# Optimization experiments

Hardware: AMD Instinct MI355X
Metric: run time of the kernel (lower is better)

Reference implementation:

```python
import jax, jax.numpy as jnp
import numpy as np

B = 65536
HID = 256
C_K, C_V, C_S, NQ = 4, 8, 4, 4
EMB_OUT = 64  # state_embedding_size - 1


def _spatial_basis():
    # h = w = 5, U = V = 2 -> [5,5,4] Fourier basis
    ph = jnp.arange(1.0, 6.0)[:, None] * jnp.ones((1, 5)) * (np.pi / 5.0)
    pw = jnp.ones((5, 1)) * jnp.arange(1.0, 6.0)[None, :] * (np.pi / 5.0)
    u = jnp.arange(1.0, 3.0)[None, :]
    a = jnp.cos(ph[:, :, None] * u)  # [5,5,2]
    b = jnp.cos(pw[:, :, None] * u)  # [5,5,2]
    return jnp.einsum('hwu,hwv->hwuv', a, b).reshape(5, 5, 4).astype(jnp.float32)


def _conv(x, w, b):
    # x: NHWC, w: HWIO, pad=1, stride=1
    y = jax.lax.conv_general_dilated(x, w, window_strides=(1, 1), padding=[(1, 1), (1, 1)],
                                     dimension_numbers=('NHWC', 'HWIO', 'NHWC'))
    return y + b


def setup_inputs() -> dict:
    key = jax.random.key(0)
    ks = jax.random.split(key, 20)
    s = 0.05
    inp = {
        'X': jax.random.normal(ks[0], (B, 7, 7, 3), jnp.float32),
        'upper_module_hidden_state': jax.random.normal(ks[1], (B, HID), jnp.float32),
        'c1_w': jax.random.normal(ks[2], (5, 5, 3, 8), jnp.float32) * s,
        'c1_b': jax.random.normal(ks[3], (8,), jnp.float32) * s,
        'c2_w': jax.random.normal(ks[4], (3, 3, 8, 12), jnp.float32) * s,
        'c2_b': jax.random.normal(ks[5], (12,), jnp.float32) * s,
    }
    qdims = [(HID, 256), (256, 128), (128, 64), (64, 32), (32, 32)]
    for i, (din, dout) in enumerate(qdims):
        inp[f'qw{i}'] = jax.random.normal(ks[6 + 2 * i], (din, dout), jnp.float32) * s
        inp[f'qb{i}'] = jax.random.normal(ks[7 + 2 * i], (dout,), jnp.float32) * s
    inp['aw0'] = jax.random.normal(ks[16], ((C_V + C_S) * NQ, 32), jnp.float32) * s
    inp['ab0'] = jax.random.normal(ks[17], (32,), jnp.float32) * s
    inp['aw1'] = jax.random.normal(ks[18], (32, EMB_OUT), jnp.float32) * s
    inp['ab1'] = jax.random.normal(ks[19], (EMB_OUT,), jnp.float32) * s
    return inp


def reference(X, upper_module_hidden_state, c1_w, c1_b, c2_w, c2_b,
              qw0, qb0, qw1, qb1, qw2, qb2, qw3, qb3, qw4, qb4,
              aw0, ab0, aw1, ab1):
    b = X.shape[0]
    # vision CNN: [b,7,7,3] -> [b,5,5,8] -> [b,5,5,12]
    O = _conv(_conv(X, c1_w, c1_b), c2_w, c2_b)
    K, V = O[..., :C_K], O[..., C_K:]
    S = jnp.broadcast_to(_spatial_basis(), (b, 5, 5, C_S))
    K = jnp.concatenate([K, S], axis=-1)  # [b,5,5,8]
    V = jnp.concatenate([V, S], axis=-1)  # [b,5,5,12]
    # query MLP -> [b,4,8]
    q = upper_module_hidden_state
    for w, bi in [(qw0, qb0), (qw1, qb1), (qw2, qb2), (qw3, qb3)]:
        q = jax.nn.relu(q @ w + bi)
    q = (q @ qw4 + qb4).reshape(-1, NQ, C_K + C_S)
    # attention logits over 25 spatial positions, softmax over space
    A = jnp.einsum('bhwk,bqk->bhwq', K, q).reshape(b, 25, NQ)
    A = jax.nn.softmax(A, axis=1)
    # apply_alpha: [b,nq,25] @ [b,25,12] -> [b,nq,12]; chunk+cat == reshape
    a = jnp.einsum('bpq,bpd->bqd', A, V.reshape(b, 25, C_V + C_S)).reshape(b, NQ * (C_V + C_S))
    # answer MLP
    return jax.nn.relu(a @ aw0 + ab0) @ aw1 + ab1
```

## Files before the change

kernel.cpp:

```cpp
#include <hip/hip_runtime.h>
#include <hip/hip_bf16.h>

#define NB 65536

typedef __attribute__((ext_vector_type(8))) short short8;
typedef __attribute__((ext_vector_type(4))) short short4v;
typedef __attribute__((ext_vector_type(4))) float f32x4;
typedef __attribute__((ext_vector_type(16))) float f32x16;
typedef __attribute__((ext_vector_type(4))) unsigned int u32x4;

__device__ inline short f2bf(float f) {
    unsigned u = __builtin_bit_cast(unsigned, f);
    unsigned r = (u + 0x7fffu + ((u >> 16) & 1u)) >> 16;
    return (short)(unsigned short)r;
}
__device__ inline float b2f(short s) {
    return __builtin_bit_cast(float, (unsigned)((unsigned short)s) << 16);
}
__device__ inline unsigned pkbf(float lo, float hi) {
    return ((unsigned)(unsigned short)f2bf(hi) << 16) | (unsigned)(unsigned short)f2bf(lo);
}

#define MLPW_CNT 109568
#define WEFF_CNT 51200
#define A0 (MLPW_CNT + WEFF_CNT + 320)
#define A1 (A0 + 2048)
#define A2 (A1 + 2048)
#define A3 (A2 + 100)
#define PREP_TOT (A3 + 512)


__global__ void __launch_bounds__(256) prep_kernel(
    const float* __restrict__ w0, const float* __restrict__ w1,
    const float* __restrict__ w2, const float* __restrict__ w3,
    const float* __restrict__ w4,
    const float* __restrict__ b0, const float* __restrict__ b1,
    const float* __restrict__ b2, const float* __restrict__ b3,
    const float* __restrict__ b4,
    const float* __restrict__ c1w, const float* __restrict__ c1b,
    const float* __restrict__ c2w, const float* __restrict__ c2b,
    const float* __restrict__ aw0, const float* __restrict__ aw1,
    short* __restrict__ wt, short* __restrict__ weff, float* __restrict__ beff,
    short* __restrict__ aw0T, short* __restrict__ aw1T, float* __restrict__ sTab,
    float* __restrict__ biasP)
{
    int idx = blockIdx.x * 256 + threadIdx.x;
    if (idx < MLPW_CNT) {
        const float* W; int N, KT, base;
        if (idx < 65536)       { W = w0; N = 256; KT = 16; base = 0; }
        else if (idx < 98304)  { W = w1; N = 128; KT = 16; base = 65536; }
        else if (idx < 106496) { W = w2; N = 64;  KT = 8;  base = 98304; }
        else if (idx < 108544) { W = w3; N = 32;  KT = 4;  base = 106496; }
        else                   { W = w4; N = 32;  KT = 2;  base = 108544; }
        int i  = idx - base;
        int nt = i / (KT * 512);
        int r1 = i - nt * (KT * 512);
        int kt = r1 >> 9;
        int l  = (r1 & 511) >> 3;
        int j  = i & 7;
        int n  = nt * 32 + (l & 31);
        int k  = kt * 16 + ((l >> 5) << 3) + j;
        wt[idx] = f2bf(W[k * N + n]);
    } else if (idx < MLPW_CNT + WEFF_CNT) {
        int it = idx - MLPW_CNT;
        int n = it / 160, k = it - n * 160;
        float acc = 0.f;
        if (n < 300 && k < 147) {
            int oc = n % 12, p = n / 12, oy = p / 5, ox = p - oy * 5;
            int ci = k % 3,  t = k / 3, iy = t / 7, ix = t - iy * 7;
            for (int y = 0; y < 5; ++y) {
                int ky = iy - y + 1, ly = y - oy + 1;
                if ((unsigned)ky < 5u && (unsigned)ly < 3u) {
                    for (int x = 0; x < 5; ++x) {
                        int kx = ix - x + 1, lx = x - ox + 1;
                        if ((unsigned)kx < 5u && (unsigned)lx < 3u) {
                            const float* p1 = c1w + ((ky * 5 + kx) * 3 + ci) * 8;
                            const float* p2 = c2w + ((ly * 3 + lx) * 8) * 12 + oc;
#pragma unroll
                            for (int c = 0; c < 8; ++c) acc += p1[c] * p2[c * 12];
                        }
                    }
                }
            }
        }
        weff[it] = f2bf(acc);
    } else if (idx < A0) {
        int n = idx - MLPW_CNT - WEFF_CNT;
        float acc = 0.f;
        if (n < 300) {
            int oc = n % 12, p = n / 12, oy = p / 5, ox = p - oy * 5;
            acc = c2b[oc];
            for (int y = 0; y < 5; ++y) {
                int ly = y - oy + 1;
                if ((unsigned)ly < 3u) {
                    for (int x = 0; x < 5; ++x) {
                        int lx = x - ox + 1;
                        if ((unsigned)lx < 3u) {
#pragma unroll
                            for (int c = 0; c < 8; ++c)
                                acc += c2w[((ly * 3 + lx) * 8 + c) * 12 + oc] * c1b[c];
                        }
                    }
                }
            }
        }
        beff[n] = acc;
    } else if (idx < A1) {
        int t = idx - A0;
        int n = t >> 6, k = t & 63;
        aw0T[t] = (k < 48) ? f2bf(aw0[k * 32 + n]) : (short)0;
    } else if (idx < A2) {
        int t = idx - A1;
        int n = t >> 5, k = t & 31;
        aw1T[t] = f2bf(aw1[k * 64 + n]);
    } else if (idx < A3) {
        int i = idx - A2;
        int p = i >> 2, s = i & 3;
        int h = p / 5, w = p - 5 * h;
        int u = (s >> 1) + 1, v = (s & 1) + 1;
        const float PI5 = 0.6283185307179586f;
        sTab[i] = cosf(((float)(h + 1) * PI5) * (float)u) *
                  cosf(((float)(w + 1) * PI5) * (float)v);
    } else if (idx < PREP_TOT) {
        int t = idx - A3;
        const float* B; int N, base;
        if (t < 256)      { B = b0; N = 256; base = 0; }
        else if (t < 384) { B = b1; N = 128; base = 256; }
        else if (t < 448) { B = b2; N = 64;  base = 384; }
        else if (t < 480) { B = b3; N = 32;  base = 448; }
        else              { B = b4; N = 32;  base = 480; }
        int u  = t - base;
        int h  = u / (N / 2);
        int w  = u - h * (N / 2);
        int nt = w >> 4, r = w & 15;
        biasP[t] = B[nt * 32 + (r & 3) + 8 * (r >> 2) + 4 * h];
    }
}

template<int K, int N, bool RELU>
__device__ inline void layerR(const short* __restrict__ wp,
                              const float* __restrict__ bp,
                              const u32x4* __restrict__ inF,
                              u32x4* __restrict__ outF,
                              int lane, int h)
{
    constexpr int KT = K / 16, NT = N / 32;
#pragma unroll
    for (int nt = 0; nt < NT; ++nt) {
        f32x16 a;
#pragma unroll
        for (int r = 0; r < 16; ++r) a[r] = 0.f;
#pragma unroll
        for (int kt = 0; kt < KT; ++kt) {
            short8 wf = *(const short8*)(wp + (nt * KT + kt) * 512 + lane * 8);
            a = __builtin_amdgcn_mfma_f32_32x32x16_bf16(
                    wf, __builtin_bit_cast(short8, inF[kt]), a, 0, 0, 0);
        }
        const float* bpp = bp + h * (N / 2) + nt * 16;
        unsigned q[8];
#pragma unroll
        for (int i = 0; i < 8; ++i) {
            float v0 = a[2 * i] + bpp[2 * i];
            float v1 = a[2 * i + 1] + bpp[2 * i + 1];
            if (RELU) { v0 = fmaxf(v0, 0.f); v1 = fmaxf(v1, 0.f); }
            q[i] = pkbf(v0, v1);
        }
        unsigned xq[8];
#pragma unroll
        for (int i = 0; i < 8; ++i) xq[i] = (unsigned)__shfl_xor((int)q[i], 32, 64);
        u32x4 fa, fb;
        if (h == 0) {
            fa[0] = q[0];  fa[1] = q[1];  fa[2] = xq[0]; fa[3] = xq[1];
            fb[0] = q[4];  fb[1] = q[5];  fb[2] = xq[4]; fb[3] = xq[5];
        } else {
            fa[0] = xq[2]; fa[1] = xq[3]; fa[2] = q[2];  fa[3] = q[3];
            fb[0] = xq[6]; fb[1] = xq[7]; fb[2] = q[6];  fb[3] = q[7];
        }
        outF[2 * nt]     = fa;
        outF[2 * nt + 1] = fb;
    }
}

template<int K>
__device__ inline void layerQ(const short* __restrict__ wp,
                              const float* __restrict__ bp,
                              const u32x4* __restrict__ inF,
                              short* __restrict__ qout,
                              int lane, int h, int r0)
{
    constexpr int KT = K / 16;
    f32x16 a;
#pragma unroll
    for (int r = 0; r < 16; ++r) a[r] = 0.f;
#pragma unroll
    for (int kt = 0; kt < KT; ++kt) {
        short8 wf = *(const short8*)(wp + kt * 512 + lane * 8);
        a = __builtin_amdgcn_mfma_f32_32x32x16_bf16(
                wf, __builtin_bit_cast(short8, inF[kt]), a, 0, 0, 0);
    }
    const float* bpp = bp + h * 16;
    short* qb = qout + (size_t)(r0 + (lane & 31)) * 32 + 4 * h;
    const int fo[8] = {0, 2, 8, 10, 16, 18, 24, 26};
#pragma unroll
    for (int i = 0; i < 8; ++i) {
        float v0 = a[2 * i] + bpp[2 * i];
        float v1 = a[2 * i + 1] + bpp[2 * i + 1];
        *(unsigned*)(qb + fo[i]) = pkbf(v0, v1);
    }
}

__global__ void __launch_bounds__(64, 2) mlp_kernel(
    const float* __restrict__ hid,
    const short* __restrict__ wp,
    const float* __restrict__ biasP,
    short* __restrict__ qout)
{
    const int lane = threadIdx.x;
    const int h = lane >> 5, b = lane & 31;
    const int r0 = blockIdx.x * 32;

    u32x4 A[16], B[16], C[8], D[4], E[2];
    const float* hb = hid + (size_t)(r0 + b) * 256 + h * 8;
#pragma unroll
    for (int kt = 0; kt < 16; ++kt) {
        float4 x = *(const float4*)(hb + kt * 16);
        float4 y = *(const float4*)(hb + kt * 16 + 4);
        u32x4 f;
        f[0] = pkbf(x.x, x.y); f[1] = pkbf(x.z, x.w);
        f[2] = pkbf(y.x, y.y); f[3] = pkbf(y.z, y.w);
        A[kt] = f;
    }
    layerR<256, 256, true>(wp,          biasP,       A, B, lane, h);
    layerR<256, 128, true>(wp + 65536,  biasP + 256, B, C, lane, h);
    layerR<128,  64, true>(wp + 98304,  biasP + 384, C, D, lane, h);
    layerR< 64,  32, true>(wp + 106496, biasP + 448, D, E, lane, h);
    layerQ< 32>           (wp + 108544, biasP + 480, E, qout, lane, h, r0);
}

__global__ void __launch_bounds__(256, 4) conv_attn_kernel(
    const float* __restrict__ Xg,
    const short* __restrict__ weffT,
    const float* __restrict__ beff,
    const short* __restrict__ aw0T, const float* __restrict__ ab0,
    const short* __restrict__ aw1T, const float* __restrict__ ab1,
    const float* __restrict__ sTab,
    const short* __restrict__ qb16,
    float* __restrict__ out)
{
    __shared__ __align__(16) short sKV[4][4800];
    __shared__ __align__(16) short sA[4][1024];
    __shared__ __align__(16) short sH[4][512];

    const int tid    = threadIdx.x;
    const int w      = tid >> 6;
    const int lane   = tid & 63;
    const int lanelo = lane & 15;
    const int g      = lane >> 4;
    const int e0     = blockIdx.x * 64 + w * 16;

    short* sX  = &sKV[w][0];
    short* sKc = &sKV[w][0];
    short* sVc = &sKV[w][1600];

#pragma unroll
    for (int i = 0; i < 4; ++i) {
        int t = lane + i * 64;
        if (t < 208) {
            int r = t / 13, c = 147 + (t - r * 13);
            int ch = c >> 3;
            sX[r * 192 + ((ch ^ (r & 7)) << 3) + (c & 7)] = 0;
        }
    }
    {
        const float* xb = Xg + (size_t)e0 * 147;
#define PUTX(IDX, F) { int _i = (IDX); int _r = _i / 147; int _c = _i - _r * 147; \
        int _ch = _c >> 3; sX[_r * 192 + ((_ch ^ (_r & 7)) << 3) + (_c & 7)] = f2bf(F); }
#pragma unroll
        for (int i = 0; i < 10; ++i) {
            int idx4 = lane + i * 64;
            if (idx4 < 588) {
                float4 v = reinterpret_cast<const float4*>(xb)[idx4];
                int base = idx4 * 4;
                PUTX(base + 0, v.x)
                PUTX(base + 1, v.y)
                PUTX(base + 2, v.z)
                PUTX(base + 3, v.w)
            }
        }
#undef PUTX
    }

    short8 af[5];
#pragma unroll
    for (int kt = 0; kt < 5; ++kt) {
        int phys = (kt * 4 + g) ^ (lanelo & 7);
        af[kt] = *(const short8*)(sX + lanelo * 192 + phys * 8);
    }

    short8 bf[3][5];
    {
        const short* wb0 = weffT + lanelo * 160 + g * 8;
        const short* wb1 = weffT + (16 + lanelo) * 160 + g * 8;
#pragma unroll
        for (int kt = 0; kt < 5; ++kt) {
            bf[0][kt] = *(const short8*)(wb0 + kt * 32);
            bf[1][kt] = *(const short8*)(wb1 + kt * 32);
        }
    }
#pragma unroll
    for (int nt = 0; nt < 19; ++nt) {
        if (nt + 2 < 19) {
            const short* wb = weffT + ((nt + 2) * 16 + lanelo) * 160 + g * 8;
#pragma unroll
            for (int kt = 0; kt < 5; ++kt)
                bf[(nt + 2) % 3][kt] = *(const short8*)(wb + kt * 32);
        }
        f32x4 a; a[0] = 0.f; a[1] = 0.f; a[2] = 0.f; a[3] = 0.f;
#pragma unroll
        for (int kt = 0; kt < 5; ++kt)
            a = __builtin_amdgcn_mfma_f32_16x16x32_bf16(af[kt], bf[nt % 3][kt], a, 0, 0, 0);
        int n = nt * 16 + lanelo;
        if (n < 300) {
            float bb = beff[n];
            int p = n / 12, c = n - p * 12;
#pragma unroll
            for (int j = 0; j < 4; ++j) {
                int el = g * 4 + j;
                float v = a[j] + bb;
                if (c < 4) sKc[el * 100 + p * 4 + c]       = f2bf(v);
                else       sVc[el * 200 + p * 8 + (c - 4)] = f2bf(v);
            }
        }
    }

    {
        const int el = lane >> 2, qi = lane & 3;
        short8 qv = *(const short8*)(qb16 + (size_t)(e0 + el) * 32 + qi * 8);
        float qf[8];
#pragma unroll
        for (int i = 0; i < 8; ++i) qf[i] = b2f(qv[i]);

        float lg[25];
        float mx = -1e30f;
#pragma unroll
        for (int p = 0; p < 25; ++p) {
            short4v kv = *(const short4v*)(sKc + el * 100 + p * 4);
            float4 sv = *(const float4*)(sTab + p * 4);
            float s = b2f(kv[0]) * qf[0] + b2f(kv[1]) * qf[1]
                    + b2f(kv[2]) * qf[2] + b2f(kv[3]) * qf[3]
                    + sv.x * qf[4] + sv.y * qf[5]
                    + sv.z * qf[6] + sv.w * qf[7];
            lg[p] = s;
            mx = fmaxf(mx, s);
        }
        float sum = 0.f;
#pragma unroll
        for (int p = 0; p < 25; ++p) { lg[p] = __expf(lg[p] - mx); sum += lg[p]; }
        float inv = 1.f / sum;

        float o[12];
#pragma unroll
        for (int d = 0; d < 12; ++d) o[d] = 0.f;
#pragma unroll
        for (int p = 0; p < 25; ++p) {
            float wgt = lg[p];
            short4v v0 = *(const short4v*)(sVc + el * 200 + p * 8);
            short4v v1 = *(const short4v*)(sVc + el * 200 + p * 8 + 4);
            float4 sv = *(const float4*)(sTab + p * 4);
            o[0] += wgt * b2f(v0[0]); o[1] += wgt * b2f(v0[1]);
            o[2] += wgt * b2f(v0[2]); o[3] += wgt * b2f(v0[3]);
            o[4] += wgt * b2f(v1[0]); o[5] += wgt * b2f(v1[1]);
            o[6] += wgt * b2f(v1[2]); o[7] += wgt * b2f(v1[3]);
            o[8]  += wgt * sv.x; o[9]  += wgt * sv.y;
            o[10] += wgt * sv.z; o[11] += wgt * sv.w;
        }
#pragma unroll
        for (int d = 0; d < 12; ++d) {
            int col = qi * 12 + d;
            int ch = col >> 3;
            sA[w][el * 64 + ((ch ^ (el & 7)) << 3) + (col & 7)] = f2bf(o[d] * inv);
        }
#pragma unroll
        for (int z = 0; z < 4; ++z) {
            int col = 48 + qi * 4 + z;
            int ch = col >> 3;
            sA[w][el * 64 + ((ch ^ (el & 7)) << 3) + (col & 7)] = 0;
        }
    }

    {
        short8 aa0, aa1;
        {
            int p0 = (0 * 4 + g) ^ (lanelo & 7);
            int p1 = (1 * 4 + g) ^ (lanelo & 7);
            aa0 = *(const short8*)(&sA[w][0] + lanelo * 64 + p0 * 8);
            aa1 = *(const short8*)(&sA[w][0] + lanelo * 64 + p1 * 8);
        }
#pragma unroll
        for (int nt2 = 0; nt2 < 2; ++nt2) {
            int n = nt2 * 16 + lanelo;
            short8 bw0 = *(const short8*)(aw0T + n * 64 + g * 8);
            short8 bw1 = *(const short8*)(aw0T + n * 64 + 32 + g * 8);
            f32x4 hh; hh[0] = 0.f; hh[1] = 0.f; hh[2] = 0.f; hh[3] = 0.f;
            hh = __builtin_amdgcn_mfma_f32_16x16x32_bf16(aa0, bw0, hh, 0, 0, 0);
            hh = __builtin_amdgcn_mfma_f32_16x16x32_bf16(aa1, bw1, hh, 0, 0, 0);
            float bb = ab0[n];
#pragma unroll
            for (int j = 0; j < 4; ++j) {
                int row = g * 4 + j;
                int ch = n >> 3;
                float v = fmaxf(hh[j] + bb, 0.f);
                sH[w][row * 32 + ((ch ^ (row & 3)) << 3) + (n & 7)] = f2bf(v);
            }
        }
    }

    {
        short8 ah;
        {
            int ph = (g ^ (lanelo & 3));
            ah = *(const short8*)(&sH[w][0] + lanelo * 32 + ph * 8);
        }
#pragma unroll
        for (int nt3 = 0; nt3 < 4; ++nt3) {
            int n = nt3 * 16 + lanelo;
            short8 bw = *(const short8*)(aw1T + n * 32 + g * 8);
            f32x4 oacc; oacc[0] = 0.f; oacc[1] = 0.f; oacc[2] = 0.f; oacc[3] = 0.f;
            oacc = __builtin_amdgcn_mfma_f32_16x16x32_bf16(ah, bw, oacc, 0, 0, 0);
            float bb = ab1[n];
#pragma unroll
            for (int j = 0; j < 4; ++j) {
                int el = g * 4 + j;
                out[((size_t)e0 + el) * 64 + n] = oacc[j] + bb;
            }
        }
    }
}


extern "C" void kernel_launch(void* const* d_in, const int* in_sizes, int n_in,
                              void* d_out, int out_size, void* d_ws, size_t ws_size,
                              hipStream_t stream)
{
    const float* X   = (const float*)d_in[0];
    const float* hid = (const float*)d_in[1];
    const float* c1w = (const float*)d_in[2];
    const float* c1b = (const float*)d_in[3];
    const float* c2w = (const float*)d_in[4];
    const float* c2b = (const float*)d_in[5];
    const float* qw0 = (const float*)d_in[6];
    const float* qb0 = (const float*)d_in[7];
    const float* qw1 = (const float*)d_in[8];
    const float* qb1 = (const float*)d_in[9];
    const float* qw2 = (const float*)d_in[10];
    const float* qb2 = (const float*)d_in[11];
    const float* qw3 = (const float*)d_in[12];
    const float* qb3 = (const float*)d_in[13];
    const float* qw4 = (const float*)d_in[14];
    const float* qb4 = (const float*)d_in[15];
    const float* aw0 = (const float*)d_in[16];
    const float* ab0 = (const float*)d_in[17];
    const float* aw1 = (const float*)d_in[18];
    const float* ab1 = (const float*)d_in[19];

    float* out   = (float*)d_out;
    short* qb16  = (short*)d_ws;
    short* wsW   = qb16 + (size_t)NB * 32;
    short* weffT = wsW + MLPW_CNT;
    float* beff  = (float*)(weffT + WEFF_CNT);
    short* aw0T  = (short*)(beff + 320);
    short* aw1T  = aw0T + 2048;
    float* sTab  = (float*)(aw1T + 2048);
    float* biasP = sTab + 100;

    hipLaunchKernelGGL(prep_kernel, dim3((PREP_TOT + 255) / 256), dim3(256), 0, stream,
                       qw0, qw1, qw2, qw3, qw4, qb0, qb1, qb2, qb3, qb4,
                       c1w, c1b, c2w, c2b, aw0, aw1,
                       wsW, weffT, beff, aw0T, aw1T, sTab, biasP);
    hipLaunchKernelGGL(mlp_kernel, dim3(NB / 32), dim3(64), 0, stream,
                       hid, wsW, biasP, qb16);
    hipLaunchKernelGGL(conv_attn_kernel, dim3(NB / 64), dim3(256), 0, stream,
                       X, weffT, beff, aw0T, ab0, aw1T, ab1, sTab, qb16, out);
}
```

Measured before the change: 82.98 us.

## Fuse query MLP and conv-attention into one warp-specialized kernel

Merges the MLP kernel and the conv/attention kernel into a single 192-thread block. One wave computes the query MLP for 32 elements and writes the queries to shared memory, while two waves run the conv path, then all three sync before attention. This removes the global round trip of the query buffer and one kernel launch, and lets MLP and conv work overlap within a block. In exchange, the MLP wave sits idle after the sync, each block carries a heavier register footprint, and blocks are smaller, which may hurt occupancy.

```diff
diff --git a/kernel.cpp b/kernel.cpp
--- a/kernel.cpp
+++ b/kernel.cpp
@@ -185,8 +185,8 @@
 __device__ inline void layerQ(const short* __restrict__ wp,
                               const float* __restrict__ bp,
                               const u32x4* __restrict__ inF,
-                              short* __restrict__ qout,
-                              int lane, int h, int r0)
+                              short* qout,
+                              int lane, int h)
 {
     constexpr int KT = K / 16;
     f32x16 a;
@@ -199,7 +199,7 @@
                 wf, __builtin_bit_cast(short8, inF[kt]), a, 0, 0, 0);
     }
     const float* bpp = bp + h * 16;
-    short* qb = qout + (size_t)(r0 + (lane & 31)) * 32 + 4 * h;
+    short* qb = qout + (lane & 31) * 32 + 4 * h;
     const int fo[8] = {0, 2, 8, 10, 16, 18, 24, 26};
 #pragma unroll
     for (int i = 0; i < 8; ++i) {
@@ -209,58 +209,56 @@
     }
 }
 
-__global__ void __launch_bounds__(64, 2) mlp_kernel(
+__global__ void __launch_bounds__(192, 4) fused_kernel(
     const float* __restrict__ hid,
     const short* __restrict__ wp,
     const float* __restrict__ biasP,
-    short* __restrict__ qout)
-{
-    const int lane = threadIdx.x;
-    const int h = lane >> 5, b = lane & 31;
-    const int r0 = blockIdx.x * 32;
-
-    u32x4 A[16], B[16], C[8], D[4], E[2];
-    const float* hb = hid + (size_t)(r0 + b) * 256 + h * 8;
-#pragma unroll
-    for (int kt = 0; kt < 16; ++kt) {
-        float4 x = *(const float4*)(hb + kt * 16);
-        float4 y = *(const float4*)(hb + kt * 16 + 4);
-        u32x4 f;
-        f[0] = pkbf(x.x, x.y); f[1] = pkbf(x.z, x.w);
-        f[2] = pkbf(y.x, y.y); f[3] = pkbf(y.z, y.w);
-        A[kt] = f;
-    }
-    layerR<256, 256, true>(wp,          biasP,       A, B, lane, h);
-    layerR<256, 128, true>(wp + 65536,  biasP + 256, B, C, lane, h);
-    layerR<128,  64, true>(wp + 98304,  biasP + 384, C, D, lane, h);
-    layerR< 64,  32, true>(wp + 106496, biasP + 448, D, E, lane, h);
-    layerQ< 32>           (wp + 108544, biasP + 480, E, qout, lane, h, r0);
-}
-
-__global__ void __launch_bounds__(256, 4) conv_attn_kernel(
     const float* __restrict__ Xg,
     const short* __restrict__ weffT,
     const float* __restrict__ beff,
     const short* __restrict__ aw0T, const float* __restrict__ ab0,
     const short* __restrict__ aw1T, const float* __restrict__ ab1,
     const float* __restrict__ sTab,
-    const short* __restrict__ qb16,
     float* __restrict__ out)
 {
-    __shared__ __align__(16) short sKV[4][4800];
-    __shared__ __align__(16) short sA[4][1024];
-    __shared__ __align__(16) short sH[4][512];
-
-    const int tid    = threadIdx.x;
-    const int w      = tid >> 6;
-    const int lane   = tid & 63;
+    __shared__ __align__(16) short sPool[2][4800];
+    __shared__ __align__(16) short sQ[1024];
+
+    const int tid  = threadIdx.x;
+    const int w    = tid / 64;
+    const int lane = tid & 63;
+    const int e0   = blockIdx.x * 32;
+
+    if (w == 0) {
+        const int h = lane >> 5, b = lane & 31;
+        u32x4 A[16], B[16], C[8], D[4], E[2];
+        const float* hb = hid + (size_t)(e0 + b) * 256 + h * 8;
+#pragma unroll
+        for (int kt = 0; kt < 16; ++kt) {
+            float4 x = *(const float4*)(hb + kt * 16);
+            float4 y = *(const float4*)(hb + kt * 16 + 4);
+            u32x4 f;
+            f[0] = pkbf(x.x, x.y); f[1] = pkbf(x.z, x.w);
+            f[2] = pkbf(y.x, y.y); f[3] = pkbf(y.z, y.w);
+            A[kt] = f;
+        }
+        layerR<256, 256, true>(wp,          biasP,       A, B, lane, h);
+        layerR<256, 128, true>(wp + 65536,  biasP + 256, B, C, lane, h);
+        layerR<128,  64, true>(wp + 98304,  biasP + 384, C, D, lane, h);
+        layerR< 64,  32, true>(wp + 106496, biasP + 448, D, E, lane, h);
+        layerQ< 32>           (wp + 108544, biasP + 480, E, sQ, lane, h);
+        __syncthreads();
+        return;
+    }
+
+    const int cw     = w - 1;
     const int lanelo = lane & 15;
     const int g      = lane >> 4;
-    const int e0     = blockIdx.x * 64 + w * 16;
-
-    short* sX  = &sKV[w][0];
-    short* sKc = &sKV[w][0];
-    short* sVc = &sKV[w][1600];
+    short* sX  = &sPool[cw][0];
+    short* sKc = &sPool[cw][0];
+    short* sVc = &sPool[cw][1600];
+    short* sAh = &sPool[cw][0];
+    short* sHh = &sPool[cw][1024];
 
 #pragma unroll
     for (int i = 0; i < 4; ++i) {
@@ -272,7 +270,7 @@
         }
     }
     {
-        const float* xb = Xg + (size_t)e0 * 147;
+        const float* xb = Xg + (size_t)(e0 + cw * 16) * 147;
 #define PUTX(IDX, F) { int _i = (IDX); int _r = _i / 147; int _c = _i - _r * 147; \
         int _ch = _c >> 3; sX[_r * 192 + ((_ch ^ (_r & 7)) << 3) + (_c & 7)] = f2bf(F); }
 #pragma unroll
@@ -333,9 +331,11 @@
         }
     }
 
+    __syncthreads();
+
     {
         const int el = lane >> 2, qi = lane & 3;
-        short8 qv = *(const short8*)(qb16 + (size_t)(e0 + el) * 32 + qi * 8);
+        short8 qv = *(const short8*)(sQ + (cw * 16 + el) * 32 + qi * 8);
         float qf[8];
 #pragma unroll
         for (int i = 0; i < 8; ++i) qf[i] = b2f(qv[i]);
@@ -378,13 +378,13 @@
         for (int d = 0; d < 12; ++d) {
             int col = qi * 12 + d;
             int ch = col >> 3;
-            sA[w][el * 64 + ((ch ^ (el & 7)) << 3) + (col & 7)] = f2bf(o[d] * inv);
+            sAh[el * 64 + ((ch ^ (el & 7)) << 3) + (col & 7)] = f2bf(o[d] * inv);
         }
 #pragma unroll
         for (int z = 0; z < 4; ++z) {
             int col = 48 + qi * 4 + z;
             int ch = col >> 3;
-            sA[w][el * 64 + ((ch ^ (el & 7)) << 3) + (col & 7)] = 0;
+            sAh[el * 64 + ((ch ^ (el & 7)) << 3) + (col & 7)] = 0;
         }
     }
 
@@ -393,8 +393,8 @@
         {
             int p0 = (0 * 4 + g) ^ (lanelo & 7);
             int p1 = (1 * 4 + g) ^ (lanelo & 7);
-            aa0 = *(const short8*)(&sA[w][0] + lanelo * 64 + p0 * 8);
-            aa1 = *(const short8*)(&sA[w][0] + lanelo * 64 + p1 * 8);
+            aa0 = *(const short8*)(sAh + lanelo * 64 + p0 * 8);
+            aa1 = *(const short8*)(sAh + lanelo * 64 + p1 * 8);
         }
 #pragma unroll
         for (int nt2 = 0; nt2 < 2; ++nt2) {
@@ -410,7 +410,7 @@
                 int row = g * 4 + j;
                 int ch = n >> 3;
                 float v = fmaxf(hh[j] + bb, 0.f);
-                sH[w][row * 32 + ((ch ^ (row & 3)) << 3) + (n & 7)] = f2bf(v);
+                sHh[row * 32 + ((ch ^ (row & 3)) << 3) + (n & 7)] = f2bf(v);
             }
         }
     }
@@ -419,7 +419,7 @@
         short8 ah;
         {
             int ph = (g ^ (lanelo & 3));
-            ah = *(const short8*)(&sH[w][0] + lanelo * 32 + ph * 8);
+            ah = *(const short8*)(sHh + lanelo * 32 + ph * 8);
         }
 #pragma unroll
         for (int nt3 = 0; nt3 < 4; ++nt3) {
@@ -431,7 +431,7 @@
 #pragma unroll
             for (int j = 0; j < 4; ++j) {
                 int el = g * 4 + j;
-                out[((size_t)e0 + el) * 64 + n] = oacc[j] + bb;
+                out[((size_t)e0 + cw * 16 + el) * 64 + n] = oacc[j] + bb;
             }
         }
     }
@@ -464,8 +464,7 @@
     const float* ab1 = (const float*)d_in[19];
 
     float* out   = (float*)d_out;
-    short* qb16  = (short*)d_ws;
-    short* wsW   = qb16 + (size_t)NB * 32;
+    short* wsW   = (short*)d_ws;
     short* weffT = wsW + MLPW_CNT;
     float* beff  = (float*)(weffT + WEFF_CNT);
     short* aw0T  = (short*)(beff + 320);
@@ -477,8 +476,7 @@
                        qw0, qw1, qw2, qw3, qw4, qb0, qb1, qb2, qb3, qb4,
                        c1w, c1b, c2w, c2b, aw0, aw1,
                        wsW, weffT, beff, aw0T, aw1T, sTab, biasP);
-    hipLaunchKernelGGL(mlp_kernel, dim3(NB / 32), dim3(64), 0, stream,
-                       hid, wsW, biasP, qb16);
-    hipLaunchKernelGGL(conv_attn_kernel, dim3(NB / 64), dim3(256), 0, stream,
-                       X, weffT, beff, aw0T, ab0, aw1T, ab1, sTab, qb16, out);
-}
+    hipLaunchKernelGGL(fused_kernel, dim3(NB / 32), dim3(192), 0, stream,
+                       hid, wsW, biasP, X, weffT, beff,
+                       aw0T, ab0, aw1T, ab1, sTab, out);
+}
```

New measurement: 141.6 us. 70.6% more time.

## Share MLP weight tiles across four waves via double-buffered LDS staging

Applied to the files above, without the earlier changes.

The MLP kernel now runs 4 waves per block, each handling 32 rows. Each layer's weight column tiles are loaded cooperatively into double-buffered shared memory and reused by all four waves, so every wave no longer fetches all weights from global/L2 itself. The next tile is prefetched into registers while the current tile's MFMAs run. The cost is a block-wide barrier per tile, 32KB of LDS, and extra register pressure that could lower occupancy.

```diff
diff --git a/kernel.cpp b/kernel.cpp
--- a/kernel.cpp
+++ b/kernel.cpp
@@ -137,22 +137,58 @@
     }
 }
 
+template<int KT>
+__device__ inline void stage_load(const short* __restrict__ src,
+                                  short8* r, int tid)
+{
+    constexpr int CNT = (KT * 64 + 255) / 256;
+#pragma unroll
+    for (int i = 0; i < CNT; ++i) {
+        int idx = tid + i * 256;
+        if (idx < KT * 64) r[i] = *(const short8*)(src + idx * 8);
+    }
+}
+template<int KT>
+__device__ inline void stage_write(short* __restrict__ dst,
+                                   const short8* r, int tid)
+{
+    constexpr int CNT = (KT * 64 + 255) / 256;
+#pragma unroll
+    for (int i = 0; i < CNT; ++i) {
+        int idx = tid + i * 256;
+        if (idx < KT * 64) *(short8*)(dst + idx * 8) = r[i];
+    }
+}
+
 template<int K, int N, bool RELU>
-__device__ inline void layerR(const short* __restrict__ wp,
+__device__ inline void layerS(const short* __restrict__ wp,
                               const float* __restrict__ bp,
                               const u32x4* __restrict__ inF,
                               u32x4* __restrict__ outF,
-                              int lane, int h)
+                              short* __restrict__ sW0,
+                              short* __restrict__ sW1,
+                              int tid, int lane, int h)
 {
     constexpr int KT = K / 16, NT = N / 32;
+    constexpr int CNT = (KT * 64 + 255) / 256;
+    short8 tmp[CNT];
+
+    stage_load<KT>(wp, tmp, tid);
+    stage_write<KT>(sW0, tmp, tid);
+    __syncthreads();
+
 #pragma unroll
     for (int nt = 0; nt < NT; ++nt) {
+        short* cur = (nt & 1) ? sW1 : sW0;
+        short* nxt = (nt & 1) ? sW0 : sW1;
+        if (nt + 1 < NT) stage_load<KT>(wp + (nt + 1) * KT * 512, tmp, tid);
+
         f32x16 a;
 #pragma unroll
         for (int r = 0; r < 16; ++r) a[r] = 0.f;
 #pragma unroll
         for (int kt = 0; kt < KT; ++kt) {
-            short8 wf = *(const short8*)(wp + (nt * KT + kt) * 512 + lane * 8);
+            short8 wf = *(const short8*)(cur + kt * 512 + lane * 8);
             a = __builtin_amdgcn_mfma_f32_32x32x16_bf16(
                     wf, __builtin_bit_cast(short8, inF[kt]), a, 0, 0, 0);
         }
@@ -178,6 +214,9 @@
         }
         outF[2 * nt]     = fa;
         outF[2 * nt + 1] = fb;
+
+        if (nt + 1 < NT) stage_write<KT>(nxt, tmp, tid);
+        __syncthreads();
     }
 }
 
@@ -209,15 +248,20 @@
     }
 }
 
-__global__ void __launch_bounds__(64, 2) mlp_kernel(
+__global__ void __launch_bounds__(256, 2) mlp_kernel(
     const float* __restrict__ hid,
     const short* __restrict__ wp,
     const float* __restrict__ biasP,
     short* __restrict__ qout)
 {
-    const int lane = threadIdx.x;
+    __shared__ __align__(16) short sW0[8192];
+    __shared__ __align__(16) short sW1[8192];
+
+    const int tid  = threadIdx.x;
+    const int lane = tid & 63;
+    const int wv   = tid >> 6;
     const int h = lane >> 5, b = lane & 31;
-    const int r0 = blockIdx.x * 32;
+    const int r0 = blockIdx.x * 128 + wv * 32;
 
     u32x4 A[16], B[16], C[8], D[4], E[2];
     const float* hb = hid + (size_t)(r0 + b) * 256 + h * 8;
@@ -230,10 +274,10 @@
         f[2] = pkbf(y.x, y.y); f[3] = pkbf(y.z, y.w);
         A[kt] = f;
     }
-    layerR<256, 256, true>(wp,          biasP,       A, B, lane, h);
-    layerR<256, 128, true>(wp + 65536,  biasP + 256, B, C, lane, h);
-    layerR<128,  64, true>(wp + 98304,  biasP + 384, C, D, lane, h);
-    layerR< 64,  32, true>(wp + 106496, biasP + 448, D, E, lane, h);
+    layerS<256, 256, true>(wp,          biasP,       A, B, sW0, sW1, tid, lane, h);
+    layerS<256, 128, true>(wp + 65536,  biasP + 256, B, C, sW0, sW1, tid, lane, h);
+    layerS<128,  64, true>(wp + 98304,  biasP + 384, C, D, sW0, sW1, tid, lane, h);
+    layerS< 64,  32, true>(wp + 106496, biasP + 448, D, E, sW0, sW1, tid, lane, h);
     layerQ< 32>           (wp + 108544, biasP + 480, E, qout, lane, h, r0);
 }
 
@@ -477,7 +521,7 @@
                        qw0, qw1, qw2, qw3, qw4, qb0, qb1, qb2, qb3, qb4,
                        c1w, c1b, c2w, c2b, aw0, aw1,
                        wsW, weffT, beff, aw0T, aw1T, sTab, biasP);
-    hipLaunchKernelGGL(mlp_kernel, dim3(NB / 32), dim3(64), 0, stream,
+    hipLaunchKernelGGL(mlp_kernel, dim3(NB / 128), dim3(256), 0, stream,
                        hid, wsW, biasP, qb16);
     hipLaunchKernelGGL(conv_attn_kernel, dim3(NB / 64), dim3(256), 0, stream,
                        X, weffT, beff, aw0T, ab0, aw1T, ab1, sTab, qb16, out);
```

New measurement: 75.74 us. -8.7%, faster.
